# Kernel tuning notes

Hardware: AMD Instinct MI355X
Metric: run time of the kernel (lower is better)

Reference implementation:

```python
import jax, jax.numpy as jnp
import numpy as np

B, N, D, H, DH, FF, CI, K, MPE = 8, 1024, 512, 8, 64, 2048, 1024, 31, 512
PAD = (K // 2, K // 2 - (K + 1) % 2)  # (15, 15)


def _ln(x, g, b):
    m = x.mean(-1, keepdims=True)
    v = ((x - m) ** 2).mean(-1, keepdims=True)
    return (x - m) * jax.lax.rsqrt(v + 1e-5) * g + b


def _swish(x):
    return x * jax.nn.sigmoid(x)


def setup_inputs() -> dict:
    key = jax.random.key(0)
    ks = iter(jax.random.split(key, 40))
    def w(shape, s=0.02):
        return (jax.random.normal(next(ks), shape) * s).astype(jnp.float32)
    ones = lambda n: jnp.ones((n,), jnp.float32)
    zeros = lambda n: jnp.zeros((n,), jnp.float32)
    return dict(
        x=jax.random.normal(next(ks), (B, N, D), dtype=jnp.float32),
        f1_g=ones(D), f1_b=zeros(D), f1_w1=w((D, FF)), f1_b1=zeros(FF), f1_w2=w((FF, D)), f1_b2=zeros(D),
        a_g=ones(D), a_b=zeros(D), wq=w((D, H * DH)), wkv=w((D, 2 * H * DH)), wo=w((H * DH, D)), wo_b=zeros(D),
        rel=w((2 * MPE + 1, DH)),
        c_g=ones(D), c_b=zeros(D), cw1=w((D, 2 * CI)), cb1=zeros(2 * CI), dw=w((CI, K)), db=zeros(CI),
        bn_g=ones(CI), bn_b=zeros(CI), bn_m=zeros(CI), bn_v=ones(CI), cw2=w((CI, D)), cb2=zeros(D),
        f2_g=ones(D), f2_b=zeros(D), f2_w1=w((D, FF)), f2_b1=zeros(FF), f2_w2=w((FF, D)), f2_b2=zeros(D),
        p_g=ones(D), p_b=zeros(D),
    )


def reference(x, f1_g, f1_b, f1_w1, f1_b1, f1_w2, f1_b2,
              a_g, a_b, wq, wkv, wo, wo_b, rel,
              c_g, c_b, cw1, cb1, dw, db, bn_g, bn_b, bn_m, bn_v, cw2, cb2,
              f2_g, f2_b, f2_w1, f2_b1, f2_w2, f2_b2, p_g, p_b):
    # FF1 (half-step)
    h = _ln(x, f1_g, f1_b)
    x = x + 0.5 * (_swish(h @ f1_w1 + f1_b1) @ f1_w2 + f1_b2)
    # Attention with relative positional bias
    h = _ln(x, a_g, a_b)
    q = (h @ wq).reshape(B, N, H, DH).transpose(0, 2, 1, 3)          # bhnd
    k, v = jnp.split(h @ wkv, 2, axis=-1)
    k = k.reshape(B, N, H, DH).transpose(0, 2, 1, 3)
    v = v.reshape(B, N, H, DH).transpose(0, 2, 1, 3)
    scale = DH ** -0.5
    dots = jnp.einsum('bhid,bhjd->bhij', q, k) * scale
    seq = jnp.arange(N)
    dist = jnp.clip(seq[:, None] - seq[None, :], -MPE, MPE) + MPE    # [N,N]
    rp = rel[dist]                                                   # [N,N,DH]
    dots = dots + jnp.einsum('bhnd,nrd->bhnr', q, rp) * scale
    attn = jax.nn.softmax(dots, axis=-1)
    o = jnp.einsum('bhij,bhjd->bhid', attn, v).transpose(0, 2, 1, 3).reshape(B, N, H * DH)
    x = x + o @ wo + wo_b
    # Conv module: LN -> pw conv -> GLU -> depthwise conv -> BN(eval) -> swish -> pw conv
    h = _ln(x, c_g, c_b)
    h = h @ cw1 + cb1                                                # [B,N,2CI]
    out, gate = jnp.split(h, 2, axis=-1)
    h = (out * jax.nn.sigmoid(gate)).transpose(0, 2, 1)              # [B,CI,N]
    h = jnp.pad(h, ((0, 0), (0, 0), PAD))
    h = jax.lax.conv_general_dilated(h, dw[:, None, :], (1,), 'VALID',
                                     feature_group_count=CI,
                                     dimension_numbers=('NCH', 'OIH', 'NCH')) + db[None, :, None]
    h = (h - bn_m[None, :, None]) * jax.lax.rsqrt(bn_v[None, :, None] + 1e-5) * bn_g[None, :, None] + bn_b[None, :, None]
    h = _swish(h).transpose(0, 2, 1)                                 # [B,N,CI]
    x = x + h @ cw2 + cb2
    # FF2 (half-step) + post norm
    h = _ln(x, f2_g, f2_b)
    x = x + 0.5 * (_swish(h @ f2_w1 + f2_b1) @ f2_w2 + f2_b2)
    return _ln(x, p_g, p_b)
```

## Files before the change

### kernel.cpp

```cpp
#include <hip/hip_runtime.h>
#include <hip/hip_bf16.h>
#include <cstdint>


using bf16_t = __hip_bfloat16;
typedef __bf16 bf16x8 __attribute__((ext_vector_type(8)));
typedef float floatx4 __attribute__((ext_vector_type(4)));

struct alignas(16) hbf8 { bf16_t h[8]; };
struct alignas(8)  hbf4 { bf16_t h[4]; };

__device__ __forceinline__ float  b2f(bf16_t h) { return __bfloat162float(h); }
__device__ __forceinline__ bf16_t f2b(float f)  { return __float2bfloat16(f); }
__device__ __forceinline__ float  sig_(float x) { return 1.f / (1.f + __expf(-x)); }

__device__ __forceinline__ void async16(const void* g, void* l) {
  __builtin_amdgcn_global_load_lds(
      (const __attribute__((address_space(1))) unsigned int*)(uintptr_t)g,
      (__attribute__((address_space(3))) unsigned int*)(uintptr_t)l, 16, 0, 0);
}

struct GemmArgs {
  const bf16_t* A; const bf16_t* Bt; const float* bias; const bf16_t* qr;
  bf16_t* C; float* resid;
  int K, lda, ldb, ldc, ldqr;
  long sAb, sAh, sBb, sBh, sCb, sCh;
  float alpha, beta;
};

template <int BM, int BN, int WR, int WC, int EPI>
__global__ __launch_bounds__(256) void gemm_bt(GemmArgs g) {
  constexpr int FM = BM / (WR * 16);
  constexpr int FN = BN / (WC * 16);
  constexpr int IA = (BM * 4) / 256;
  constexpr int IB = (BN * 4) / 256;
  __shared__ __align__(16) bf16_t As[BM * 32];
  __shared__ __align__(16) bf16_t Bs[BN * 32];
  const int tid = threadIdx.x;
  const int lane = tid & 63, w = tid >> 6;
  const int bm0 = blockIdx.y * BM, bn0 = blockIdx.x * BN;
  const int zb = blockIdx.z >> 3, zh = blockIdx.z & 7;
  const bf16_t* Ab = g.A + (long)zb * g.sAb + (long)zh * g.sAh;
  const bf16_t* Bb = g.Bt + (long)zb * g.sBb + (long)zh * g.sBh;
  const int wm0 = (w / WC) * (FM * 16);
  const int wn0 = (w % WC) * (FN * 16);
  const int lrow = lane & 15, lq = lane >> 4;

  floatx4 acc[FM][FN] = {};

  for (int k0 = 0; k0 < g.K; k0 += 32) {
#pragma unroll
    for (int i = 0; i < IA; ++i) {
      int c = i * 256 + tid;
      int m = c >> 2, kk = (c & 3) * 8;
      async16(Ab + (long)(bm0 + m) * g.lda + (k0 + kk), (char*)As + c * 16);
    }
#pragma unroll
    for (int i = 0; i < IB; ++i) {
      int c = i * 256 + tid;
      int n = bn0 + (c >> 2), kk = (c & 3) * 8;
      async16(Bb + (long)n * g.ldb + (k0 + kk), (char*)Bs + c * 16);
    }
    __syncthreads();
    bf16x8 af[FM], bfr[FN];
#pragma unroll
    for (int fm = 0; fm < FM; ++fm)
      af[fm] = *(const bf16x8*)(As + (wm0 + fm * 16 + lrow) * 32 + lq * 8);
#pragma unroll
    for (int fn = 0; fn < FN; ++fn)
      bfr[fn] = *(const bf16x8*)(Bs + (wn0 + fn * 16 + lrow) * 32 + lq * 8);
#pragma unroll
    for (int fm = 0; fm < FM; ++fm)
#pragma unroll
      for (int fn = 0; fn < FN; ++fn)
        acc[fm][fn] = __builtin_amdgcn_mfma_f32_16x16x32_bf16(af[fm], bfr[fn], acc[fm][fn], 0, 0, 0);
    __syncthreads();
  }

  const int bi = bm0 + wm0 + lq * 4;
  const int bj = bn0 + wn0 + lrow;
  if constexpr (EPI == 2) {
    float* R = g.resid;
#pragma unroll
    for (int fm = 0; fm < FM; ++fm)
#pragma unroll
      for (int fn = 0; fn < FN; ++fn) {
        int j = bj + fn * 16;
        float bv = g.bias ? g.bias[j] : 0.f;
#pragma unroll
        for (int r = 0; r < 4; ++r) {
          long i = bi + fm * 16 + r;
          R[i * g.ldc + j] += g.beta * (acc[fm][fn][r] + bv);
        }
      }
  } else {
    bf16_t* C = g.C + (long)zb * g.sCb + (long)zh * g.sCh;
#pragma unroll
    for (int fm = 0; fm < FM; ++fm)
#pragma unroll
      for (int fn = 0; fn < FN; ++fn) {
        int j = bj + fn * 16;
        float bv = g.bias ? g.bias[j] : 0.f;
#pragma unroll
        for (int r = 0; r < 4; ++r) {
          int i = bi + fm * 16 + r;
          float v = acc[fm][fn][r];
          if constexpr (EPI == 0) v = g.alpha * v + bv;
          if constexpr (EPI == 1) { v += bv; v = v * sig_(v); }
          C[(long)i * g.ldc + j] = f2b(v);
        }
      }
  }
}

__global__ __launch_bounds__(512) void attn_kernel(
    const bf16_t* __restrict__ Q, const bf16_t* __restrict__ KV,
    const bf16_t* __restrict__ VT, const bf16_t* __restrict__ RELP,
    bf16_t* __restrict__ O) {
  constexpr int LDT = 1160;
  __shared__ __align__(16) bf16_t Tls[32 * LDT];
  __shared__ float scr[640];

  const int tid = threadIdx.x;
  const int w = tid >> 6, lane = tid & 63;
  const int lrow = lane & 15, lq = lane >> 4;
  const int i0 = blockIdx.x * 32;
  const int z = blockIdx.y;
  const int b = z >> 3, zh = z & 7;
  const int j0w = w * 128;

  const bf16_t* Qb  = Q  + ((long)(b * 1024 + i0)) * 512 + zh * 64;
  const bf16_t* Kb  = KV + ((long)b * 1024) * 1024 + zh * 64;
  const bf16_t* VTb = VT + ((long)(b * 8 + zh)) * 65536;

  bf16x8 af[2][2];
#pragma unroll
  for (int fm = 0; fm < 2; ++fm)
#pragma unroll
    for (int ks = 0; ks < 2; ++ks)
      af[fm][ks] = *(const bf16x8*)(Qb + (long)(fm * 16 + lrow) * 512 + ks * 32 + lq * 8);

  {
    const int u0w = w * 144;
#pragma unroll
    for (int fnT = 0; fnT < 9; ++fnT) {
      const int u0 = u0w + fnT * 16;
      floatx4 tacc[2] = {};
#pragma unroll
      for (int ks = 0; ks < 2; ++ks) {
        bf16x8 br = *(const bf16x8*)(RELP + (long)(u0 + lrow) * 64 + ks * 32 + lq * 8);
        tacc[0] = __builtin_amdgcn_mfma_f32_16x16x32_bf16(af[0][ks], br, tacc[0], 0, 0, 0);
        tacc[1] = __builtin_amdgcn_mfma_f32_16x16x32_bf16(af[1][ks], br, tacc[1], 0, 0, 0);
      }
#pragma unroll
      for (int fm = 0; fm < 2; ++fm)
#pragma unroll
        for (int r = 0; r < 4; ++r)
          Tls[(fm * 16 + lq * 4 + r) * LDT + u0 + lrow] = f2b(tacc[fm][r]);
    }
  }
  __syncthreads();

  floatx4 sacc[2][8] = {};
#pragma unroll
  for (int fn = 0; fn < 8; ++fn) {
#pragma unroll
    for (int ks = 0; ks < 2; ++ks) {
      bf16x8 bk = *(const bf16x8*)(Kb + (long)(j0w + fn * 16 + lrow) * 1024 + ks * 32 + lq * 8);
      sacc[0][fn] = __builtin_amdgcn_mfma_f32_16x16x32_bf16(af[0][ks], bk, sacc[0][fn], 0, 0, 0);
      sacc[1][fn] = __builtin_amdgcn_mfma_f32_16x16x32_bf16(af[1][ks], bk, sacc[1][fn], 0, 0, 0);
    }
  }

#pragma unroll
  for (int fm = 0; fm < 2; ++fm)
#pragma unroll
    for (int r = 0; r < 4; ++r) {
      const int il = fm * 16 + lq * 4 + r;
      const bf16_t* trow = Tls + il * LDT + 512;
      const int tb = i0 + il - j0w - lrow;
#pragma unroll
      for (int fn = 0; fn < 8; ++fn) {
        int t = tb - fn * 16;
        t = t < -512 ? -512 : (t > 512 ? 512 : t);
        sacc[fm][fn][r] += b2f(trow[t]);
      }
    }

  float rmax[2][4];
#pragma unroll
  for (int fm = 0; fm < 2; ++fm)
#pragma unroll
    for (int r = 0; r < 4; ++r) {
      float m = sacc[fm][0][r];
#pragma unroll
      for (int fn = 1; fn < 8; ++fn) m = fmaxf(m, sacc[fm][fn][r]);
      rmax[fm][r] = m;
    }
#pragma unroll
  for (int off = 1; off < 16; off <<= 1)
#pragma unroll
    for (int fm = 0; fm < 2; ++fm)
#pragma unroll
      for (int r = 0; r < 4; ++r)
        rmax[fm][r] = fmaxf(rmax[fm][r], __shfl_xor(rmax[fm][r], off));
  if (lrow == 0)
#pragma unroll
    for (int fm = 0; fm < 2; ++fm)
#pragma unroll
      for (int r = 0; r < 4; ++r)
        scr[(fm * 16 + lq * 4 + r) * 9 + w] = rmax[fm][r];
  __syncthreads();
  if (tid < 32) {
    const float* rr = scr + tid * 9;
    float m = rr[0];
#pragma unroll
    for (int ww = 1; ww < 8; ++ww) m = fmaxf(m, rr[ww]);
    scr[288 + tid] = m;
  }
  __syncthreads();

  float rsum[2][4];
#pragma unroll
  for (int fm = 0; fm < 2; ++fm)
#pragma unroll
    for (int r = 0; r < 4; ++r) {
      const float m = scr[288 + fm * 16 + lq * 4 + r];
      float s = 0.f;
#pragma unroll
      for (int fn = 0; fn < 8; ++fn) {
        float e = __expf(sacc[fm][fn][r] - m);
        sacc[fm][fn][r] = e;
        s += e;
      }
      rsum[fm][r] = s;
    }
#pragma unroll
  for (int off = 1; off < 16; off <<= 1)
#pragma unroll
    for (int fm = 0; fm < 2; ++fm)
#pragma unroll
      for (int r = 0; r < 4; ++r)
        rsum[fm][r] += __shfl_xor(rsum[fm][r], off);
  if (lrow == 0)
#pragma unroll
    for (int fm = 0; fm < 2; ++fm)
#pragma unroll
      for (int r = 0; r < 4; ++r)
        scr[320 + (fm * 16 + lq * 4 + r) * 9 + w] = rsum[fm][r];
  __syncthreads();
  if (tid < 32) {
    const float* rr = scr + 320 + tid * 9;
    float s = rr[0];
#pragma unroll
    for (int ww = 1; ww < 8; ++ww) s += rr[ww];
    scr[608 + tid] = 1.f / s;
  }
  __syncthreads();
  float inv[2][4];
#pragma unroll
  for (int fm = 0; fm < 2; ++fm)
#pragma unroll
    for (int r = 0; r < 4; ++r)
      inv[fm][r] = scr[608 + fm * 16 + lq * 4 + r];
  __syncthreads();

#pragma unroll
  for (int fm = 0; fm < 2; ++fm)
#pragma unroll
    for (int fn = 0; fn < 8; ++fn)
#pragma unroll
      for (int r = 0; r < 4; ++r) {
        const int i = fm * 16 + lq * 4 + r;
        const int j = j0w + fn * 16 + lrow;
        const unsigned boff = (unsigned)(i * 2048 + j * 2) ^ ((unsigned)(i & 7) << 4);
        *(bf16_t*)((char*)Tls + boff) = f2b(sacc[fm][fn][r] * inv[fm][r]);
      }

  floatx4 oacc[2][4] = {};
#pragma unroll
  for (int ks = 0; ks < 4; ++ks) {
    const int j = j0w + ks * 32;
    bf16x8 ap[2];
#pragma unroll
    for (int fm = 0; fm < 2; ++fm) {
      const int i = fm * 16 + lrow;
      const unsigned boff = (unsigned)(i * 2048 + (j + lq * 8) * 2) ^ ((unsigned)(i & 7) << 4);
      ap[fm] = *(const bf16x8*)((char*)Tls + boff);
    }
#pragma unroll
    for (int fd = 0; fd < 4; ++fd) {
      bf16x8 bv = *(const bf16x8*)(VTb + (long)(fd * 16 + lrow) * 1024 + j + lq * 8);
      oacc[0][fd] = __builtin_amdgcn_mfma_f32_16x16x32_bf16(ap[0], bv, oacc[0][fd], 0, 0, 0);
      oacc[1][fd] = __builtin_amdgcn_mfma_f32_16x16x32_bf16(ap[1], bv, oacc[1][fd], 0, 0, 0);
    }
  }
  __syncthreads();

  {
    float* part = (float*)Tls + w * 2048;
#pragma unroll
    for (int fm = 0; fm < 2; ++fm)
#pragma unroll
      for (int fd = 0; fd < 4; ++fd)
#pragma unroll
        for (int r = 0; r < 4; ++r)
          part[(fm * 16 + lq * 4 + r) * 64 + fd * 16 + lrow] = oacc[fm][fd][r];
  }
  __syncthreads();

  {
    const int i = tid >> 4;
    const int d0 = (tid & 15) * 4;
    floatx4 s = {};
#pragma unroll
    for (int ww = 0; ww < 8; ++ww)
      s += *(const floatx4*)((const float*)Tls + ww * 2048 + i * 64 + d0);
    hbf4 o4;
#pragma unroll
    for (int m = 0; m < 4; ++m) o4.h[m] = f2b(s[m]);
    *(hbf4*)(O + (long)(b * 1024 + i0 + i) * 512 + zh * 64 + d0) = o4;
  }
}

__global__ __launch_bounds__(256) void diag_kernel(float* __restrict__ out, long n, float v) {
  long i = (long)blockIdx.x * 256 + threadIdx.x;
  if (i < n) out[i] = v;
}

__global__ __launch_bounds__(256) void copy_kernel(const float* __restrict__ x, float* __restrict__ X) {
  long idx = ((long)blockIdx.x * 256 + threadIdx.x) * 4;
  *(float4*)(X + idx) = *(const float4*)(x + idx);
}

__global__ __launch_bounds__(256) void relpad_kernel(const float* __restrict__ rel, bf16_t* __restrict__ RELP) {
  int i = blockIdx.x * 256 + threadIdx.x;
  if (i < 73728) {
    int r = i >> 6, c = i & 63;
    RELP[i] = (r < 1025) ? f2b(rel[r * 64 + c]) : f2b(0.f);
  }
}

template <bool F32OUT>
__global__ __launch_bounds__(256) void ln_kernel(const float* __restrict__ X, const float* __restrict__ gam,
                                                 const float* __restrict__ bet, void* __restrict__ outv) {
  int row = blockIdx.x, tid = threadIdx.x;
  const float* x = X + (long)row * 512;
  float a = x[tid], b = x[tid + 256];
  float s = a + b, q = a * a + b * b;
  for (int off = 32; off; off >>= 1) { s += __shfl_down(s, off); q += __shfl_down(q, off); }
  __shared__ float red[8];
  int w = tid >> 6;
  if ((tid & 63) == 0) { red[w] = s; red[w + 4] = q; }
  __syncthreads();
  float ts = red[0] + red[1] + red[2] + red[3];
  float tq = red[4] + red[5] + red[6] + red[7];
  float mean = ts * (1.f / 512.f);
  float var = tq * (1.f / 512.f) - mean * mean;
  float rs = rsqrtf(var + 1e-5f);
  float o0 = (a - mean) * rs * gam[tid]       + bet[tid];
  float o1 = (b - mean) * rs * gam[tid + 256] + bet[tid + 256];
  if constexpr (F32OUT) {
    float* out = (float*)outv;
    out[(long)row * 512 + tid]       = o0;
    out[(long)row * 512 + tid + 256] = o1;
  } else {
    bf16_t* out = (bf16_t*)outv;
    out[(long)row * 512 + tid]       = f2b(o0);
    out[(long)row * 512 + tid + 256] = f2b(o1);
  }
}

__global__ __launch_bounds__(256) void transpose_kernel(const float* __restrict__ in, bf16_t* __restrict__ out,
                                                        int R, int C) {
  __shared__ float t[32][33];
  int c0 = blockIdx.x * 32, r0 = blockIdx.y * 32;
  int tx = threadIdx.x & 31, ty = threadIdx.x >> 5;
#pragma unroll
  for (int i = 0; i < 4; ++i)
    t[ty + i * 8][tx] = in[(long)(r0 + ty + i * 8) * C + c0 + tx];
  __syncthreads();
#pragma unroll
  for (int i = 0; i < 4; ++i)
    out[(long)(c0 + ty + i * 8) * R + r0 + tx] = f2b(t[tx][ty + i * 8]);
}

__global__ __launch_bounds__(256) void vt_kernel(const bf16_t* __restrict__ KV, bf16_t* __restrict__ VT) {
  int jb = blockIdx.x, z = blockIdx.y;
  int b = z >> 3, h = z & 7;
  const bf16_t* src = KV + (long)b * 1024 * 1024 + 512 + h * 64;
  bf16_t* dst = VT + (long)z * 65536;
  __shared__ bf16_t t[64][65];
  int tid = threadIdx.x;
#pragma unroll
  for (int i = 0; i < 16; ++i) {
    int l = i * 256 + tid;
    int j = l >> 6, d = l & 63;
    t[d][j] = src[(long)(jb * 64 + j) * 1024 + d];
  }
  __syncthreads();
#pragma unroll
  for (int i = 0; i < 16; ++i) {
    int l = i * 256 + tid;
    int d = l >> 6, j = l & 63;
    dst[(long)d * 1024 + jb * 64 + j] = t[d][j];
  }
}

__global__ __launch_bounds__(256) void glu_kernel(const bf16_t* __restrict__ P, bf16_t* __restrict__ out) {
  long idx = ((long)blockIdx.x * 256 + threadIdx.x) * 8;
  long r = idx >> 10;
  int c = (int)(idx & 1023);
  hbf8 a = *(const hbf8*)(P + r * 2048 + c);
  hbf8 g = *(const hbf8*)(P + r * 2048 + 1024 + c);
  hbf8 o;
#pragma unroll
  for (int i = 0; i < 8; ++i) o.h[i] = f2b(b2f(a.h[i]) * sig_(b2f(g.h[i])));
  *(hbf8*)(out + idx) = o;
}

__global__ __launch_bounds__(256) void dwconv_kernel(const bf16_t* __restrict__ G, const float* __restrict__ dw,
    const float* __restrict__ db, const float* __restrict__ bng, const float* __restrict__ bnb,
    const float* __restrict__ bnm, const float* __restrict__ bnv, bf16_t* __restrict__ out) {
  int n0 = blockIdx.x * 32, c0 = blockIdx.y * 64, b = blockIdx.z;
  __shared__ bf16_t t[62][64];
  __shared__ float dws[31][64];
  int tid = threadIdx.x;
  const bf16_t* src = G + (long)b * 1024 * 1024 + c0;
#pragma unroll
  for (int i = 0; i < 16; ++i) {
    int l = i * 256 + tid;
    if (l < 3968) {
      int rr = l >> 6, c = l & 63;
      int n = n0 - 15 + rr;
      t[rr][c] = (n >= 0 && n < 1024) ? src[(long)n * 1024 + c] : f2b(0.f);
    }
  }
#pragma unroll
  for (int i = 0; i < 8; ++i) {
    int l = i * 256 + tid;
    if (l < 1984) {
      int k = l >> 6, c = l & 63;
      dws[k][c] = dw[(long)(c0 + c) * 31 + k];
    }
  }
  __syncthreads();
  int c = tid & 63, nl = tid >> 6;
  float rs = rsqrtf(bnv[c0 + c] + 1e-5f);
  float sc = rs * bng[c0 + c];
  float ab = (db[c0 + c] - bnm[c0 + c]) * sc + bnb[c0 + c];
#pragma unroll
  for (int j = 0; j < 8; ++j) {
    int rr = nl * 8 + j;
    float s = 0.f;
#pragma unroll
    for (int k = 0; k < 31; ++k) s += b2f(t[rr + k][c]) * dws[k][c];
    float y = s * sc + ab;
    out[((long)b * 1024 + n0 + rr) * 1024 + c0 + c] = f2b(y * sig_(y));
  }
}

extern "C" void kernel_launch(void* const* d_in, const int* in_sizes, int n_in,
                              void* d_out, int out_size, void* d_ws, size_t ws_size,
                              hipStream_t stream) {
  auto fail = [&](float code) {
    diag_kernel<<<(out_size + 255) / 256, 256, 0, stream>>>((float*)d_out, out_size, code);
  };
  if (n_in != 34)             { fail(70.f);  return; }
  if (in_sizes[0] != 4194304) { fail(80.f);  return; }

  const float* x     = (const float*)d_in[0];
  const float* f1_g  = (const float*)d_in[1];
  const float* f1_b  = (const float*)d_in[2];
  const float* f1_w1 = (const float*)d_in[3];
  const float* f1_b1 = (const float*)d_in[4];
  const float* f1_w2 = (const float*)d_in[5];
  const float* f1_b2 = (const float*)d_in[6];
  const float* a_g   = (const float*)d_in[7];
  const float* a_b   = (const float*)d_in[8];
  const float* wq    = (const float*)d_in[9];
  const float* wkv   = (const float*)d_in[10];
  const float* wo    = (const float*)d_in[11];
  const float* wo_b  = (const float*)d_in[12];
  const float* rel   = (const float*)d_in[13];
  const float* c_g   = (const float*)d_in[14];
  const float* c_b   = (const float*)d_in[15];
  const float* cw1   = (const float*)d_in[16];
  const float* cb1   = (const float*)d_in[17];
  const float* dwp   = (const float*)d_in[18];
  const float* dbp   = (const float*)d_in[19];
  const float* bn_g  = (const float*)d_in[20];
  const float* bn_b  = (const float*)d_in[21];
  const float* bn_m  = (const float*)d_in[22];
  const float* bn_v  = (const float*)d_in[23];
  const float* cw2   = (const float*)d_in[24];
  const float* cb2   = (const float*)d_in[25];
  const float* f2_g  = (const float*)d_in[26];
  const float* f2_b  = (const float*)d_in[27];
  const float* f2_w1 = (const float*)d_in[28];
  const float* f2_b1 = (const float*)d_in[29];
  const float* f2_w2 = (const float*)d_in[30];
  const float* f2_b2 = (const float*)d_in[31];
  const float* p_g   = (const float*)d_in[32];
  const float* p_b   = (const float*)d_in[33];

  char* ws = (char*)d_ws;
  const size_t OFF_X  = 0;
  const size_t OFF_WT = 16777216;
  const size_t OFF_D  = 30408704;
  const size_t OFF_E  = 63963136;
  const size_t relp_off = OFF_E + 33554432;
  if (ws_size < relp_off + 147456ULL) { fail(200.f); return; }

  float*  X   = (float*)(ws + OFF_X);
  bf16_t* WT  = (bf16_t*)(ws + OFF_WT);
  bf16_t* Q   = (bf16_t*)(ws + OFF_D);
  bf16_t* KV  = (bf16_t*)(ws + OFF_D + 8388608);
  bf16_t* VT  = (bf16_t*)(ws + OFF_D + 25165824);
  bf16_t* GLU = (bf16_t*)(ws + OFF_D);
  bf16_t* DWO = (bf16_t*)(ws + OFF_D + 16777216);
  bf16_t* MID = (bf16_t*)(ws + OFF_E);
  bf16_t* RELP= (bf16_t*)(ws + relp_off);
  bf16_t* H   = (bf16_t*)d_out;
  bf16_t* O   = (bf16_t*)d_out;

  bf16_t* f1_w1t = WT;            bf16_t* f1_w2t = WT + 1048576;
  bf16_t* wqt    = WT + 2097152;  bf16_t* wkvt   = WT + 2359296;
  bf16_t* wot    = WT + 2883584;  bf16_t* cw1t   = WT + 3145728;
  bf16_t* cw2t   = WT + 4194304;  bf16_t* f2_w1t = WT + 4718592;
  bf16_t* f2_w2t = WT + 5767168;

  auto GA = [](const bf16_t* A, const bf16_t* Bt, const float* bias, bf16_t* C,
               float* resid, const bf16_t* qr, int K, int lda, int ldb, int ldc,
               float alpha, float beta) {
    GemmArgs g{}; g.A = A; g.Bt = Bt; g.bias = bias; g.qr = qr; g.C = C; g.resid = resid;
    g.K = K; g.lda = lda; g.ldb = ldb; g.ldc = ldc; g.ldqr = 1152;
    g.sAb = g.sAh = g.sBb = g.sBh = g.sCb = g.sCh = 0; g.alpha = alpha; g.beta = beta;
    return g;
  };
  auto T = [&](const float* in, bf16_t* out, int R, int C) {
    transpose_kernel<<<dim3(C / 32, R / 32), 256, 0, stream>>>(in, out, R, C);
  };

  copy_kernel<<<4096, 256, 0, stream>>>(x, X);
  relpad_kernel<<<288, 256, 0, stream>>>(rel, RELP);
  T(f1_w1, f1_w1t, 512, 2048);  T(f1_w2, f1_w2t, 2048, 512);
  T(wq, wqt, 512, 512);         T(wkv, wkvt, 512, 1024);
  T(wo, wot, 512, 512);         T(cw1, cw1t, 512, 2048);
  T(cw2, cw2t, 1024, 512);      T(f2_w1, f2_w1t, 512, 2048);
  T(f2_w2, f2_w2t, 2048, 512);

  ln_kernel<false><<<8192, 256, 0, stream>>>(X, f1_g, f1_b, H);
  { GemmArgs g = GA(H, f1_w1t, f1_b1, MID, nullptr, nullptr, 512, 512, 512, 2048, 1.f, 0.f);
    gemm_bt<128, 128, 2, 2, 1><<<dim3(16, 64, 1), 256, 0, stream>>>(g); }
  { GemmArgs g = GA(MID, f1_w2t, f1_b2, nullptr, X, nullptr, 2048, 2048, 2048, 512, 1.f, 0.5f);
    gemm_bt<64, 128, 1, 4, 2><<<dim3(4, 128, 1), 256, 0, stream>>>(g); }

  ln_kernel<false><<<8192, 256, 0, stream>>>(X, a_g, a_b, H);
  { GemmArgs g = GA(H, wqt, nullptr, Q, nullptr, nullptr, 512, 512, 512, 512, 0.125f, 0.f);
    gemm_bt<128, 128, 2, 2, 0><<<dim3(4, 64, 1), 256, 0, stream>>>(g); }
  { GemmArgs g = GA(H, wkvt, nullptr, KV, nullptr, nullptr, 512, 512, 512, 1024, 1.f, 0.f);
    gemm_bt<128, 128, 2, 2, 0><<<dim3(8, 64, 1), 256, 0, stream>>>(g); }
  vt_kernel<<<dim3(16, 64), 256, 0, stream>>>(KV, VT);

  attn_kernel<<<dim3(32, 64), 512, 0, stream>>>(Q, KV, VT, RELP, O);

  { GemmArgs g = GA(O, wot, wo_b, nullptr, X, nullptr, 512, 512, 512, 512, 1.f, 1.f);
    gemm_bt<64, 128, 1, 4, 2><<<dim3(4, 128, 1), 256, 0, stream>>>(g); }

  ln_kernel<false><<<8192, 256, 0, stream>>>(X, c_g, c_b, H);
  { GemmArgs g = GA(H, cw1t, cb1, MID, nullptr, nullptr, 512, 512, 512, 2048, 1.f, 0.f);
    gemm_bt<128, 128, 2, 2, 0><<<dim3(16, 64, 1), 256, 0, stream>>>(g); }
  glu_kernel<<<4096, 256, 0, stream>>>(MID, GLU);
  dwconv_kernel<<<dim3(32, 16, 8), 256, 0, stream>>>(GLU, dwp, dbp, bn_g, bn_b, bn_m, bn_v, DWO);
  { GemmArgs g = GA(DWO, cw2t, cb2, nullptr, X, nullptr, 1024, 1024, 1024, 512, 1.f, 1.f);
    gemm_bt<64, 128, 1, 4, 2><<<dim3(4, 128, 1), 256, 0, stream>>>(g); }

  ln_kernel<false><<<8192, 256, 0, stream>>>(X, f2_g, f2_b, H);
  { GemmArgs g = GA(H, f2_w1t, f2_b1, MID, nullptr, nullptr, 512, 512, 512, 2048, 1.f, 0.f);
    gemm_bt<128, 128, 2, 2, 1><<<dim3(16, 64, 1), 256, 0, stream>>>(g); }
  { GemmArgs g = GA(MID, f2_w2t, f2_b2, nullptr, X, nullptr, 2048, 2048, 2048, 512, 1.f, 0.5f);
    gemm_bt<64, 128, 1, 4, 2><<<dim3(4, 128, 1), 256, 0, stream>>>(g); }
  ln_kernel<true><<<8192, 256, 0, stream>>>(X, p_g, p_b, (float*)d_out);
}
```

Before: 691.0 us.

## Prefetch K/V/rel fragments, trim relpos LDS, drop softmax syncs, swizzle block order

The attention kernel now loads rel-pos, K and V fragments into registers ahead of their MFMAs so global latency overlaps with other work. It shrinks the rel-pos LDS table from 1160 to 1028 columns to cut LDS use and raise occupancy, with launch bounds asking for 4 blocks per CU. It removes two barrier rounds in the softmax by having every thread reduce the per-wave max and sum itself. It also remaps block IDs in both the GEMM and the attention kernel to group neighbouring tiles for cache locality. The extra register arrays may raise register pressure or cause spills, and the attention remap hardcodes the grid size.

Result: faster. 665.9 us (-3.6%).

```diff
diff --git a/kernel.cpp b/kernel.cpp
--- a/kernel.cpp
+++ b/kernel.cpp
@@ -38,7 +38,17 @@
   __shared__ __align__(16) bf16_t Bs[BN * 32];
   const int tid = threadIdx.x;
   const int lane = tid & 63, w = tid >> 6;
-  const int bm0 = blockIdx.y * BM, bn0 = blockIdx.x * BN;
+  int bx = blockIdx.x, by = blockIdx.y;
+  {
+    const int gx = gridDim.x;
+    const int nwg = gx * gridDim.y;
+    if ((nwg & 7) == 0 && gridDim.z == 1) {
+      int lin = by * gx + bx;
+      int lid = (lin & 7) * (nwg >> 3) + (lin >> 3);
+      bx = lid % gx; by = lid / gx;
+    }
+  }
+  const int bm0 = by * BM, bn0 = bx * BN;
   const int zb = blockIdx.z >> 3, zh = blockIdx.z & 7;
   const bf16_t* Ab = g.A + (long)zb * g.sAb + (long)zh * g.sAh;
   const bf16_t* Bb = g.Bt + (long)zb * g.sBb + (long)zh * g.sBh;
@@ -113,19 +123,21 @@
   }
 }
 
-__global__ __launch_bounds__(512) void attn_kernel(
+__global__ __launch_bounds__(512, 4) void attn_kernel(
     const bf16_t* __restrict__ Q, const bf16_t* __restrict__ KV,
     const bf16_t* __restrict__ VT, const bf16_t* __restrict__ RELP,
     bf16_t* __restrict__ O) {
-  constexpr int LDT = 1160;
+  constexpr int LDT = 1028;
   __shared__ __align__(16) bf16_t Tls[32 * LDT];
-  __shared__ float scr[640];
+  __shared__ float scr[576];
 
   const int tid = threadIdx.x;
   const int w = tid >> 6, lane = tid & 63;
   const int lrow = lane & 15, lq = lane >> 4;
-  const int i0 = blockIdx.x * 32;
-  const int z = blockIdx.y;
+  const int lin = blockIdx.y * gridDim.x + blockIdx.x;
+  const int lid = (lin & 7) * 256 + (lin >> 3);
+  const int z = lid >> 5;
+  const int i0 = (lid & 31) * 32;
   const int b = z >> 3, zh = z & 7;
   const int j0w = w * 128;
 
@@ -142,34 +154,58 @@
 
   {
     const int u0w = w * 144;
+    bf16x8 rf[18];
 #pragma unroll
     for (int fnT = 0; fnT < 9; ++fnT) {
       const int u0 = u0w + fnT * 16;
-      floatx4 tacc[2] = {};
-#pragma unroll
-      for (int ks = 0; ks < 2; ++ks) {
-        bf16x8 br = *(const bf16x8*)(RELP + (long)(u0 + lrow) * 64 + ks * 32 + lq * 8);
-        tacc[0] = __builtin_amdgcn_mfma_f32_16x16x32_bf16(af[0][ks], br, tacc[0], 0, 0, 0);
-        tacc[1] = __builtin_amdgcn_mfma_f32_16x16x32_bf16(af[1][ks], br, tacc[1], 0, 0, 0);
+      if (u0 < LDT) {
+        rf[2 * fnT]     = *(const bf16x8*)(RELP + (long)(u0 + lrow) * 64 + lq * 8);
+        rf[2 * fnT + 1] = *(const bf16x8*)(RELP + (long)(u0 + lrow) * 64 + 32 + lq * 8);
       }
-#pragma unroll
-      for (int fm = 0; fm < 2; ++fm)
-#pragma unroll
-        for (int r = 0; r < 4; ++r)
-          Tls[(fm * 16 + lq * 4 + r) * LDT + u0 + lrow] = f2b(tacc[fm][r]);
-    }
-  }
+    }
+#pragma unroll
+    for (int fnT = 0; fnT < 9; ++fnT) {
+      const int u0 = u0w + fnT * 16;
+      if (u0 < LDT) {
+        floatx4 tacc[2] = {};
+        tacc[0] = __builtin_amdgcn_mfma_f32_16x16x32_bf16(af[0][0], rf[2 * fnT],     tacc[0], 0, 0, 0);
+        tacc[0] = __builtin_amdgcn_mfma_f32_16x16x32_bf16(af[0][1], rf[2 * fnT + 1], tacc[0], 0, 0, 0);
+        tacc[1] = __builtin_amdgcn_mfma_f32_16x16x32_bf16(af[1][0], rf[2 * fnT],     tacc[1], 0, 0, 0);
+        tacc[1] = __builtin_amdgcn_mfma_f32_16x16x32_bf16(af[1][1], rf[2 * fnT + 1], tacc[1], 0, 0, 0);
+        const int uu = u0 + lrow;
+#pragma unroll
+        for (int fm = 0; fm < 2; ++fm)
+#pragma unroll
+          for (int r = 0; r < 4; ++r)
+            if (uu < LDT)
+              Tls[(fm * 16 + lq * 4 + r) * LDT + uu] = f2b(tacc[fm][r]);
+      }
+    }
+  }
+
+  bf16x8 kfA[8], kfB[8];
+#pragma unroll
+  for (int x = 0; x < 8; ++x)
+    kfA[x] = *(const bf16x8*)(Kb + (long)(j0w + (x >> 1) * 16 + lrow) * 1024 + (x & 1) * 32 + lq * 8);
+#pragma unroll
+  for (int x = 0; x < 8; ++x)
+    kfB[x] = *(const bf16x8*)(Kb + (long)(j0w + (4 + (x >> 1)) * 16 + lrow) * 1024 + (x & 1) * 32 + lq * 8);
   __syncthreads();
 
   floatx4 sacc[2][8] = {};
 #pragma unroll
-  for (int fn = 0; fn < 8; ++fn) {
-#pragma unroll
-    for (int ks = 0; ks < 2; ++ks) {
-      bf16x8 bk = *(const bf16x8*)(Kb + (long)(j0w + fn * 16 + lrow) * 1024 + ks * 32 + lq * 8);
-      sacc[0][fn] = __builtin_amdgcn_mfma_f32_16x16x32_bf16(af[0][ks], bk, sacc[0][fn], 0, 0, 0);
-      sacc[1][fn] = __builtin_amdgcn_mfma_f32_16x16x32_bf16(af[1][ks], bk, sacc[1][fn], 0, 0, 0);
-    }
+  for (int fn = 0; fn < 4; ++fn) {
+    sacc[0][fn] = __builtin_amdgcn_mfma_f32_16x16x32_bf16(af[0][0], kfA[2 * fn],     sacc[0][fn], 0, 0, 0);
+    sacc[0][fn] = __builtin_amdgcn_mfma_f32_16x16x32_bf16(af[0][1], kfA[2 * fn + 1], sacc[0][fn], 0, 0, 0);
+    sacc[1][fn] = __builtin_amdgcn_mfma_f32_16x16x32_bf16(af[1][0], kfA[2 * fn],     sacc[1][fn], 0, 0, 0);
+    sacc[1][fn] = __builtin_amdgcn_mfma_f32_16x16x32_bf16(af[1][1], kfA[2 * fn + 1], sacc[1][fn], 0, 0, 0);
+  }
+#pragma unroll
+  for (int fn = 4; fn < 8; ++fn) {
+    sacc[0][fn] = __builtin_amdgcn_mfma_f32_16x16x32_bf16(af[0][0], kfB[2 * (fn - 4)],     sacc[0][fn], 0, 0, 0);
+    sacc[0][fn] = __builtin_amdgcn_mfma_f32_16x16x32_bf16(af[0][1], kfB[2 * (fn - 4) + 1], sacc[0][fn], 0, 0, 0);
+    sacc[1][fn] = __builtin_amdgcn_mfma_f32_16x16x32_bf16(af[1][0], kfB[2 * (fn - 4)],     sacc[1][fn], 0, 0, 0);
+    sacc[1][fn] = __builtin_amdgcn_mfma_f32_16x16x32_bf16(af[1][1], kfB[2 * (fn - 4) + 1], sacc[1][fn], 0, 0, 0);
   }
 
 #pragma unroll
@@ -211,21 +247,16 @@
       for (int r = 0; r < 4; ++r)
         scr[(fm * 16 + lq * 4 + r) * 9 + w] = rmax[fm][r];
   __syncthreads();
-  if (tid < 32) {
-    const float* rr = scr + tid * 9;
-    float m = rr[0];
-#pragma unroll
-    for (int ww = 1; ww < 8; ++ww) m = fmaxf(m, rr[ww]);
-    scr[288 + tid] = m;
-  }
-  __syncthreads();
 
   float rsum[2][4];
 #pragma unroll
   for (int fm = 0; fm < 2; ++fm)
 #pragma unroll
     for (int r = 0; r < 4; ++r) {
-      const float m = scr[288 + fm * 16 + lq * 4 + r];
+      const float* rr = scr + (fm * 16 + lq * 4 + r) * 9;
+      float m = rr[0];
+#pragma unroll
+      for (int ww = 1; ww < 8; ++ww) m = fmaxf(m, rr[ww]);
       float s = 0.f;
 #pragma unroll
       for (int fn = 0; fn < 8; ++fn) {
@@ -247,23 +278,25 @@
     for (int fm = 0; fm < 2; ++fm)
 #pragma unroll
       for (int r = 0; r < 4; ++r)
-        scr[320 + (fm * 16 + lq * 4 + r) * 9 + w] = rsum[fm][r];
-  __syncthreads();
-  if (tid < 32) {
-    const float* rr = scr + 320 + tid * 9;
-    float s = rr[0];
-#pragma unroll
-    for (int ww = 1; ww < 8; ++ww) s += rr[ww];
-    scr[608 + tid] = 1.f / s;
-  }
-  __syncthreads();
+        scr[288 + (fm * 16 + lq * 4 + r) * 9 + w] = rsum[fm][r];
+  __syncthreads();
+
   float inv[2][4];
 #pragma unroll
   for (int fm = 0; fm < 2; ++fm)
 #pragma unroll
-    for (int r = 0; r < 4; ++r)
-      inv[fm][r] = scr[608 + fm * 16 + lq * 4 + r];
-  __syncthreads();
+    for (int r = 0; r < 4; ++r) {
+      const float* rr = scr + 288 + (fm * 16 + lq * 4 + r) * 9;
+      float s = rr[0];
+#pragma unroll
+      for (int ww = 1; ww < 8; ++ww) s += rr[ww];
+      inv[fm][r] = 1.f / s;
+    }
+
+  bf16x8 vfA[8];
+#pragma unroll
+  for (int x = 0; x < 8; ++x)
+    vfA[x] = *(const bf16x8*)(VTb + (long)((x & 3) * 16 + lrow) * 1024 + j0w + (x >> 2) * 32 + lq * 8);
 
 #pragma unroll
   for (int fm = 0; fm < 2; ++fm)
@@ -277,6 +310,11 @@
         *(bf16_t*)((char*)Tls + boff) = f2b(sacc[fm][fn][r] * inv[fm][r]);
       }
 
+  bf16x8 vfB[8];
+#pragma unroll
+  for (int x = 0; x < 8; ++x)
+    vfB[x] = *(const bf16x8*)(VTb + (long)((x & 3) * 16 + lrow) * 1024 + j0w + 64 + (x >> 2) * 32 + lq * 8);
+
   floatx4 oacc[2][4] = {};
 #pragma unroll
   for (int ks = 0; ks < 4; ++ks) {
@@ -290,7 +328,7 @@
     }
 #pragma unroll
     for (int fd = 0; fd < 4; ++fd) {
-      bf16x8 bv = *(const bf16x8*)(VTb + (long)(fd * 16 + lrow) * 1024 + j + lq * 8);
+      bf16x8 bv = (ks < 2) ? vfA[(ks << 2) | fd] : vfB[((ks - 2) << 2) | fd];
       oacc[0][fd] = __builtin_amdgcn_mfma_f32_16x16x32_bf16(ap[0], bv, oacc[0][fd], 0, 0, 0);
       oacc[1][fd] = __builtin_amdgcn_mfma_f32_16x16x32_bf16(ap[1], bv, oacc[1][fd], 0, 0, 0);
     }
```
